# Kernel optimization log

Measured on AMD Instinct MI355X. Metric: run time of the kernel, lower is better.

The kernel has to match this reference:

```python
import jax, jax.numpy as jnp
import numpy as np

EPS = 1e-06

def rmsnorm(x, w):
    x32 = x.astype(jnp.float32)
    var = jnp.mean(x32 * x32, axis=-1, keepdims=True)
    return w * (x32 * jax.lax.rsqrt(var + EPS)).astype(x.dtype)

def setup_inputs() -> dict:
    B, T, C = 16, 256, 16
    token_dim, text_dim = 1024, 512
    key = jax.random.key(0)
    ks = jax.random.split(key, 8)
    token_embeds = jax.random.normal(ks[0], (B, T, token_dim), dtype=jnp.float32)
    char_embeds = jax.random.normal(ks[1], (B, T, C, text_dim), dtype=jnp.float32)
    filler_embed = jax.random.normal(ks[2], (text_dim,), dtype=jnp.float32)
    mask = jax.random.randint(ks[3], (B, T, C), 0, 2).astype(bool)
    mask = mask.at[0].set(True)  # force max valid count == T*C (static output shape)
    token_ids_mask = jnp.ones((B, T), dtype=bool)
    # xavier-uniform-ish weights
    def xav(k, fan_out, fan_in, gain=1.0):
        lim = gain * np.sqrt(6.0 / (fan_in + fan_out))
        return jax.random.uniform(k, (fan_out, fan_in), jnp.float32, -lim, lim)
    W_down = xav(ks[4], text_dim, token_dim)
    W_proj = xav(ks[5], 3, text_dim, gain=0.2)
    W_fusion = xav(ks[6], text_dim, text_dim)
    w_pre = jnp.ones((token_dim,), jnp.float32)
    w_tok = jnp.ones((text_dim,), jnp.float32)
    w_char = jnp.ones((text_dim,), jnp.float32)
    return {"token_embeds": token_embeds, "token_ids_mask": token_ids_mask,
            "char_embeds": char_embeds, "char_ids_mask": mask,
            "filler_embed": filler_embed, "w_pre": w_pre, "w_tok": w_tok,
            "w_char": w_char, "W_down": W_down, "W_proj": W_proj,
            "W_fusion": W_fusion, "max_valid_chars": T * C}

def reference(token_embeds, token_ids_mask, char_embeds, char_ids_mask,
              filler_embed, w_pre, w_tok, w_char, W_down, W_proj, W_fusion,
              max_valid_chars):
    B, T, C, d = char_embeds.shape
    MV = int(max_valid_chars)
    tok = rmsnorm(token_embeds, w_pre)                       # [B,T,token_dim]
    feats = rmsnorm(jnp.einsum('btk,dk->btd', tok, W_down), w_tok)  # [B,T,d]
    params = jnp.einsum('btd,pd->btp', jax.nn.silu(feats), W_proj)  # [B,T,3]
    scale = params[..., 0][:, :, None, None]                 # [B,T,1,1]
    shift = params[..., 1][:, :, None, None]
    gate = jax.nn.sigmoid(params[..., 2][:, :, None, None])
    cn = rmsnorm(char_embeds, w_char)                        # [B,T,C,d]
    fused = jnp.einsum('btcd,ed->btce', jax.nn.silu(cn * (1.0 + scale) + shift), W_fusion)
    fused = gate * fused + (1.0 - gate) * cn                 # [B,T,C,d]
    flat = fused.reshape(B, T * C, d)
    m = char_ids_mask.reshape(B, T * C).astype(jnp.int32)
    pos = jnp.cumsum(m, axis=1) - 1                          # dest within row
    offs = jnp.arange(B, dtype=jnp.int32)[:, None] * MV
    idx = jnp.where(m > 0, offs + pos, B * MV)               # invalid -> dump slot
    buf = jnp.broadcast_to(filler_embed, (B * MV + 1, d))
    buf = buf.at[idx.reshape(-1)].set(flat.reshape(-1, d))
    return buf[: B * MV].reshape(B, MV, d)
```

## Files before the change

kernel.cpp:

```cpp
#include <hip/hip_runtime.h>
#include <cstdint>
#include <cstddef>

#define EPS 1e-6f

typedef short bf16x8 __attribute__((ext_vector_type(8)));
typedef float f32x4  __attribute__((ext_vector_type(4)));

__device__ __forceinline__ short f2bf(float x) {
    uint32_t u = __builtin_bit_cast(uint32_t, x);
    return (short)((u + 0x7FFFu + ((u >> 16) & 1u)) >> 16);
}

__global__ __launch_bounds__(1024) void k_scan(const void* __restrict__ maskp,
                                               int* __restrict__ v_list,
                                               int* __restrict__ counts) {
    __shared__ int wtot[16];
    __shared__ int woff[16];
    __shared__ int mode_s;
    const int tid = threadIdx.x, lane = tid & 63, wave = tid >> 6;
    const int b = blockIdx.x;

    if (tid == 0) mode_s = 0;
    __syncthreads();
    {
        const int bad = (((const uint32_t*)maskp)[tid & 1023] > 1u) ? 1 : 0;
        if (bad) mode_s = 1;
    }
    __syncthreads();
    const int byte_mode = mode_s;

    int f0, f1, f2, f3;
    if (byte_mode) {
        const uint32_t v = ((const uint32_t*)maskp)[(b << 10) + tid];
        f0 = (v & 0x000000ffu) != 0;
        f1 = (v & 0x0000ff00u) != 0;
        f2 = (v & 0x00ff0000u) != 0;
        f3 = (v & 0xff000000u) != 0;
    } else {
        const uint4 v = ((const uint4*)maskp)[(b << 10) + tid];
        f0 = v.x != 0; f1 = v.y != 0; f2 = v.z != 0; f3 = v.w != 0;
    }
    const int c = f0 + f1 + f2 + f3;

    int incl = c;
#pragma unroll
    for (int off = 1; off < 64; off <<= 1) {
        const int n = __shfl_up(incl, off);
        if (lane >= off) incl += n;
    }
    if (lane == 63) wtot[wave] = incl;
    __syncthreads();
    if (tid == 0) {
        int run = 0;
#pragma unroll
        for (int wv = 0; wv < 16; ++wv) { woff[wv] = run; run += wtot[wv]; }
        counts[b] = run;
    }
    __syncthreads();

    int base = woff[wave] + incl - c;
    const int i0 = tid * 4;
    int* vl = v_list + (b << 12);
    if (f0) vl[base++] = i0;
    if (f1) vl[base++] = i0 + 1;
    if (f2) vl[base++] = i0 + 2;
    if (f3) vl[base++] = i0 + 3;
}

__global__ __launch_bounds__(256) void k_conv2(const float* __restrict__ srcA,
                                               short* __restrict__ dstA, int n4a,
                                               const float* __restrict__ srcB,
                                               short* __restrict__ dstB, int n4b) {
    const int gid = blockIdx.x * 256 + threadIdx.x;
    const float* s;
    short* d;
    int i;
    if (gid < n4a) { s = srcA; d = dstA; i = gid; }
    else {
        i = gid - n4a;
        if (i >= n4b) return;
        s = srcB; d = dstB;
    }
    const float4 v = ((const float4*)s)[i];
    short4 o;
    o.x = f2bf(v.x); o.y = f2bf(v.y); o.z = f2bf(v.z); o.w = f2bf(v.w);
    ((short4*)d)[i] = o;
}

__global__ __launch_bounds__(256) void k_tokprep(const float* __restrict__ tokens,
                                                 const float* __restrict__ w_pre,
                                                 short* __restrict__ tokbf) {
    const int tid = threadIdx.x, lane = tid & 63, wave = tid >> 6;
    const int row = blockIdx.x * 4 + wave;
    const float* xp = tokens + (size_t)row * 1024 + lane * 16;
    float4 x[4];
#pragma unroll
    for (int q = 0; q < 4; ++q) x[q] = *(const float4*)&xp[q * 4];
    float ss = 0.f;
#pragma unroll
    for (int q = 0; q < 4; ++q)
        ss += x[q].x * x[q].x + x[q].y * x[q].y + x[q].z * x[q].z + x[q].w * x[q].w;
#pragma unroll
    for (int off = 32; off > 0; off >>= 1) ss += __shfl_down(ss, off);
    ss = __shfl(ss, 0);
    const float r = rsqrtf(ss * (1.0f / 1024.0f) + EPS);
    const float* wp = w_pre + lane * 16;
    short* op = tokbf + (size_t)row * 1024 + lane * 16;
#pragma unroll
    for (int h = 0; h < 2; ++h) {
        bf16x8 o;
#pragma unroll
        for (int q = 0; q < 2; ++q) {
            const float4 wv = *(const float4*)&wp[h * 8 + q * 4];
            const float4 xv = x[h * 2 + q];
            o[q * 4 + 0] = f2bf(xv.x * wv.x * r);
            o[q * 4 + 1] = f2bf(xv.y * wv.y * r);
            o[q * 4 + 2] = f2bf(xv.z * wv.z * r);
            o[q * 4 + 3] = f2bf(xv.w * wv.w * r);
        }
        *(bf16x8*)&op[h * 8] = o;
    }
}

__global__ __launch_bounds__(256) void k_gemm_tok(const short* __restrict__ tokbf,
                                                  const short* __restrict__ Wdbf,
                                                  float* __restrict__ feats) {
    __shared__ short As[128 * 32];
    __shared__ short Bs[128 * 32];
    const int tid = threadIdx.x, lane = tid & 63, w = tid >> 6;
    const int kt = blockIdx.x >> 7;
    const int mt = (blockIdx.x >> 2) & 31, nt = blockIdx.x & 3;
    const int wm = w >> 1, wn = w & 1;
    const int kbase = kt * 512;
    const short* hA = tokbf + (size_t)mt * 128 * 1024;
    const short* wB = Wdbf + (size_t)nt * 128 * 1024;

    f32x4 acc[4][4];
#pragma unroll
    for (int mi = 0; mi < 4; ++mi)
#pragma unroll
        for (int ni = 0; ni < 4; ++ni) acc[mi][ni] = (f32x4)0.f;

    const int rA = lane & 15, q8 = (lane >> 4) * 8;
    for (int kk = 0; kk < 512; kk += 32) {
#pragma unroll
        for (int q = 0; q < 2; ++q) {
            const int cid = (w * 2 + q) * 64 + lane;
            const int r = cid >> 2, kc = cid & 3;
            const size_t go = (size_t)r * 1024 + kbase + kk + kc * 8;
            __builtin_amdgcn_global_load_lds(
                (const __attribute__((address_space(1))) uint32_t*)(hA + go),
                (__attribute__((address_space(3))) uint32_t*)&As[(w * 2 + q) * 512], 16, 0, 0);
            __builtin_amdgcn_global_load_lds(
                (const __attribute__((address_space(1))) uint32_t*)(wB + go),
                (__attribute__((address_space(3))) uint32_t*)&Bs[(w * 2 + q) * 512], 16, 0, 0);
        }
        __syncthreads();
        bf16x8 af[4], bfr[4];
#pragma unroll
        for (int mi = 0; mi < 4; ++mi)
            af[mi] = *(const bf16x8*)&As[(wm * 64 + mi * 16 + rA) * 32 + q8];
#pragma unroll
        for (int ni = 0; ni < 4; ++ni)
            bfr[ni] = *(const bf16x8*)&Bs[(wn * 64 + ni * 16 + rA) * 32 + q8];
#pragma unroll
        for (int mi = 0; mi < 4; ++mi)
#pragma unroll
            for (int ni = 0; ni < 4; ++ni)
                acc[mi][ni] = __builtin_amdgcn_mfma_f32_16x16x32_bf16(af[mi], bfr[ni], acc[mi][ni], 0, 0, 0);
        __syncthreads();
    }
    float* fo = feats + (size_t)kt * 4096 * 512;
    const int rowb = mt * 128 + wm * 64 + (lane >> 4) * 4;
    const int colb = nt * 128 + wn * 64 + (lane & 15);
#pragma unroll
    for (int mi = 0; mi < 4; ++mi)
#pragma unroll
        for (int ni = 0; ni < 4; ++ni)
#pragma unroll
            for (int rg = 0; rg < 4; ++rg)
                fo[(size_t)(rowb + mi * 16 + rg) * 512 + colb + ni * 16] = acc[mi][ni][rg];
}

__global__ __launch_bounds__(64) void k_params(
    const float* __restrict__ feats_pre, const float* __restrict__ w_tok,
    const float* __restrict__ W_proj, float* __restrict__ params) {
    const int tk = blockIdx.x;
    const int lane = threadIdx.x;
    const int d0 = lane * 8;
    const float* fp0 = feats_pre + (size_t)tk * 512 + d0;
    const float* fp1 = fp0 + (size_t)4096 * 512;
    const float4 a0 = *(const float4*)&fp0[0];
    const float4 a1 = *(const float4*)&fp0[4];
    const float4 b0 = *(const float4*)&fp1[0];
    const float4 b1 = *(const float4*)&fp1[4];
    const float4 f0 = make_float4(a0.x + b0.x, a0.y + b0.y, a0.z + b0.z, a0.w + b0.w);
    const float4 f1 = make_float4(a1.x + b1.x, a1.y + b1.y, a1.z + b1.z, a1.w + b1.w);
    float ss = f0.x * f0.x + f0.y * f0.y + f0.z * f0.z + f0.w * f0.w
             + f1.x * f1.x + f1.y * f1.y + f1.z * f1.z + f1.w * f1.w;
#pragma unroll
    for (int off = 32; off > 0; off >>= 1) ss += __shfl_down(ss, off);
    ss = __shfl(ss, 0);
    const float rms = rsqrtf(ss * (1.0f / 512.0f) + EPS);

    const float4 wt0 = *(const float4*)&w_tok[d0];
    const float4 wt1 = *(const float4*)&w_tok[d0 + 4];
    float fv[8] = {f0.x, f0.y, f0.z, f0.w, f1.x, f1.y, f1.z, f1.w};
    float wv[8] = {wt0.x, wt0.y, wt0.z, wt0.w, wt1.x, wt1.y, wt1.z, wt1.w};
    float s[8];
#pragma unroll
    for (int j = 0; j < 8; ++j) {
        const float v = fv[j] * wv[j] * rms;
        s[j] = v / (1.0f + expf(-v));
    }
    float p[3];
#pragma unroll
    for (int q = 0; q < 3; ++q) {
        const float* Wp = W_proj + (size_t)q * 512 + d0;
        const float4 a = *(const float4*)&Wp[0];
        const float4 c = *(const float4*)&Wp[4];
        p[q] = s[0] * a.x + s[1] * a.y + s[2] * a.z + s[3] * a.w
             + s[4] * c.x + s[5] * c.y + s[6] * c.z + s[7] * c.w;
#pragma unroll
        for (int off = 32; off > 0; off >>= 1) p[q] += __shfl_down(p[q], off);
    }
    if (lane == 0) {
        float* po = params + (size_t)tk * 4;
        po[0] = 1.0f + p[0];
        po[1] = p[1];
        po[2] = 1.0f / (1.0f + expf(-p[2]));
    }
}

__global__ __launch_bounds__(256) void k_prep(
    const float* __restrict__ chars, const float* __restrict__ w_char,
    const float* __restrict__ params, const int* __restrict__ v_list,
    const int* __restrict__ counts, short* __restrict__ hb,
    float* __restrict__ rms_l, float* __restrict__ g_l) {
    const int tid = threadIdx.x, lane = tid & 63, wave = tid >> 6;
    const int b = blockIdx.x >> 10;
    const int j = (blockIdx.x & 1023) * 4 + wave;
    const int cnt = counts[b];
    const int cpad = (cnt + 127) & ~127;
    if (j >= cpad) return;
    short* hrow = hb + ((size_t)(b << 12) + j) * 512 + lane * 8;
    if (j >= cnt) {
        *(bf16x8*)hrow = (bf16x8)0;
        return;
    }
    const int i = v_list[(b << 12) + j];
    const float* xp = chars + ((size_t)(b << 12) + i) * 512 + lane * 8;
    const float4 x0 = *(const float4*)&xp[0];
    const float4 x1 = *(const float4*)&xp[4];
    float ss = x0.x * x0.x + x0.y * x0.y + x0.z * x0.z + x0.w * x0.w
             + x1.x * x1.x + x1.y * x1.y + x1.z * x1.z + x1.w * x1.w;
#pragma unroll
    for (int off = 32; off > 0; off >>= 1) ss += __shfl_down(ss, off);
    ss = __shfl(ss, 0);
    const float rms = rsqrtf(ss * (1.0f / 512.0f) + EPS);
    const float* pp = params + (size_t)((b << 8) + (i >> 4)) * 4;
    const float s1 = pp[0], sh = pp[1], g = pp[2];
    const float4 w0 = *(const float4*)&w_char[lane * 8];
    const float4 w1 = *(const float4*)&w_char[lane * 8 + 4];
    float xv[8] = {x0.x, x0.y, x0.z, x0.w, x1.x, x1.y, x1.z, x1.w};
    float wv[8] = {w0.x, w0.y, w0.z, w0.w, w1.x, w1.y, w1.z, w1.w};
    bf16x8 o;
#pragma unroll
    for (int q = 0; q < 8; ++q) {
        const float cn = wv[q] * xv[q] * rms;
        const float a = cn * s1 + sh;
        o[q] = f2bf(a / (1.0f + expf(-a)));
    }
    *(bf16x8*)hrow = o;
    if (lane == 0) {
        rms_l[(b << 12) + j] = rms;
        g_l[(b << 12) + j] = g;
    }
}

__global__ __launch_bounds__(256) void k_gemm_fus(
    const short* __restrict__ hb, const short* __restrict__ Wbf,
    const float* __restrict__ chars, const float* __restrict__ w_char,
    const float* __restrict__ rms_l, const float* __restrict__ g_l,
    const int* __restrict__ v_list, const int* __restrict__ counts,
    const float* __restrict__ filler, float* __restrict__ out) {
    __shared__ short As[128 * 32];
    __shared__ short Bs[128 * 32];
    __shared__ float g_s[128], rms_s[128];
    __shared__ int idx_s[128];
    const int tid = threadIdx.x, lane = tid & 63, w = tid >> 6;
    const int b = blockIdx.x >> 7;
    const int mt = (blockIdx.x >> 2) & 31;
    const int nt = blockIdx.x & 3;
    const int cnt = counts[b];
    const int row0 = mt * 128;
    if (row0 >= cnt) {
        const int colb = nt * 128;
        const float4 f = ((const float4*)(filler + colb))[tid & 31];
        float* o0 = out + ((size_t)(b << 12) + row0) * 512 + colb + (tid & 31) * 4;
#pragma unroll
        for (int r = (tid >> 5); r < 128; r += 8)
            *(float4*)&o0[(size_t)r * 512] = f;
        return;
    }
    const int wm = w >> 1, wn = w & 1;

    if (tid < 128) {
        const int j = row0 + tid;
        const bool valid = j < cnt;
        idx_s[tid] = valid ? v_list[(b << 12) + j] : 0;
        g_s[tid]   = valid ? g_l[(b << 12) + j] : 0.f;
        rms_s[tid] = valid ? rms_l[(b << 12) + j] : 0.f;
    }

    const short* hA = hb + ((size_t)(b << 12) + row0) * 512;
    const short* wB = Wbf + (size_t)nt * 128 * 512;

    f32x4 acc[4][4];
#pragma unroll
    for (int mi = 0; mi < 4; ++mi)
#pragma unroll
        for (int ni = 0; ni < 4; ++ni) acc[mi][ni] = (f32x4)0.f;

    const int rA = lane & 15, q8 = (lane >> 4) * 8;
    for (int kk = 0; kk < 512; kk += 32) {
#pragma unroll
        for (int q = 0; q < 2; ++q) {
            const int cid = (w * 2 + q) * 64 + lane;
            const int r = cid >> 2, kc = cid & 3;
            const size_t go = (size_t)r * 512 + kk + kc * 8;
            __builtin_amdgcn_global_load_lds(
                (const __attribute__((address_space(1))) uint32_t*)(hA + go),
                (__attribute__((address_space(3))) uint32_t*)&As[(w * 2 + q) * 512], 16, 0, 0);
            __builtin_amdgcn_global_load_lds(
                (const __attribute__((address_space(1))) uint32_t*)(wB + go),
                (__attribute__((address_space(3))) uint32_t*)&Bs[(w * 2 + q) * 512], 16, 0, 0);
        }
        __syncthreads();
        bf16x8 af[4], bfr[4];
#pragma unroll
        for (int mi = 0; mi < 4; ++mi)
            af[mi] = *(const bf16x8*)&As[(wm * 64 + mi * 16 + rA) * 32 + q8];
#pragma unroll
        for (int ni = 0; ni < 4; ++ni)
            bfr[ni] = *(const bf16x8*)&Bs[(wn * 64 + ni * 16 + rA) * 32 + q8];
#pragma unroll
        for (int mi = 0; mi < 4; ++mi)
#pragma unroll
            for (int ni = 0; ni < 4; ++ni)
                acc[mi][ni] = __builtin_amdgcn_mfma_f32_16x16x32_bf16(af[mi], bfr[ni], acc[mi][ni], 0, 0, 0);
        __syncthreads();
    }

    const int colb = nt * 128 + wn * 64 + (lane & 15);
    float wcv[4];
#pragma unroll
    for (int ni = 0; ni < 4; ++ni) wcv[ni] = w_char[colb + ni * 16];
#pragma unroll
    for (int mi = 0; mi < 4; ++mi) {
#pragma unroll
        for (int rg = 0; rg < 4; ++rg) {
            const int jl = wm * 64 + mi * 16 + (lane >> 4) * 4 + rg;
            const int j = row0 + jl;
            const size_t orow = ((size_t)(b << 12) + j) * 512;
            if (j < cnt) {
                const float g = g_s[jl], rm = rms_s[jl];
                const size_t xrow = ((size_t)(b << 12) + idx_s[jl]) * 512;
#pragma unroll
                for (int ni = 0; ni < 4; ++ni) {
                    const int col = colb + ni * 16;
                    const float x = chars[xrow + col];
                    const float cn = wcv[ni] * x * rm;
                    out[orow + col] = g * acc[mi][ni][rg] + (1.0f - g) * cn;
                }
            } else {
#pragma unroll
                for (int ni = 0; ni < 4; ++ni) {
                    const int col = colb + ni * 16;
                    out[orow + col] = filler[col];
                }
            }
        }
    }
}

extern "C" void kernel_launch(void* const* d_in, const int* in_sizes, int n_in,
                              void* d_out, int out_size, void* d_ws, size_t ws_size,
                              hipStream_t stream) {
    const float* tokens = (const float*)d_in[0];
    const float* chars  = (const float*)d_in[2];
    const void*  cmask  = d_in[3];
    const float* filler = (const float*)d_in[4];
    const float* w_pre  = (const float*)d_in[5];
    const float* w_tok  = (const float*)d_in[6];
    const float* w_char = (const float*)d_in[7];
    const float* W_down = (const float*)d_in[8];
    const float* W_proj = (const float*)d_in[9];
    const float* W_fus  = (const float*)d_in[10];
    float* out = (float*)d_out;

    float* feats_pre = (float*)d_ws;
    float* params    = feats_pre + (size_t)2 * 4096 * 512;
    int*   counts    = (int*)(params + (size_t)4096 * 4);
    int*   v_list    = counts + 16;
    float* rms_l     = (float*)(v_list + 65536);
    float* g_l       = rms_l + 65536;
    short* Wbf       = (short*)(g_l + 65536);
    short* hb        = Wbf + (size_t)512 * 512;
    short* tokbf     = hb + (size_t)16 * 4096 * 512;
    short* Wdbf      = tokbf + (size_t)4096 * 1024;

    k_scan<<<16, 1024, 0, stream>>>(cmask, v_list, counts);
    k_conv2<<<768, 256, 0, stream>>>(W_fus, Wbf, 65536, W_down, Wdbf, 131072);
    k_tokprep<<<1024, 256, 0, stream>>>(tokens, w_pre, tokbf);
    k_gemm_tok<<<256, 256, 0, stream>>>(tokbf, Wdbf, feats_pre);
    k_params<<<4096, 64, 0, stream>>>(feats_pre, w_tok, W_proj, params);
    k_prep<<<16384, 256, 0, stream>>>(chars, w_char, params, v_list, counts, hb, rms_l, g_l);
    k_gemm_fus<<<2048, 256, 0, stream>>>(hb, Wbf, chars, w_char, rms_l, g_l, v_list, counts, filler, out);
}
```

Baseline: 339.8 us.

## Merge front kernels, swizzle GEMM LDS tiles, remap fusion blocks, use nontemporal stores

Folds the mask scan, weight bf16 conversion and token RMSNorm into one launch, cutting two kernel launches. It also adds an XOR swizzle to the LDS tile layout in both GEMMs to reduce bank conflicts on fragment reads. The fusion GEMM's block index is remapped so blocks are interleaved across XCDs, and output/filler writes become nontemporal stores to avoid cache pollution. The scan now uses 256 threads with 16 elements each, and params gets an explicit zero in its fourth slot.

```diff
diff --git a/kernel.cpp b/kernel.cpp
--- a/kernel.cpp
+++ b/kernel.cpp
@@ -12,114 +12,111 @@
     return (short)((u + 0x7FFFu + ((u >> 16) & 1u)) >> 16);
 }
 
-__global__ __launch_bounds__(1024) void k_scan(const void* __restrict__ maskp,
-                                               int* __restrict__ v_list,
-                                               int* __restrict__ counts) {
-    __shared__ int wtot[16];
-    __shared__ int woff[16];
-    __shared__ int mode_s;
-    const int tid = threadIdx.x, lane = tid & 63, wave = tid >> 6;
-    const int b = blockIdx.x;
-
-    if (tid == 0) mode_s = 0;
-    __syncthreads();
-    {
-        const int bad = (((const uint32_t*)maskp)[tid & 1023] > 1u) ? 1 : 0;
-        if (bad) mode_s = 1;
-    }
-    __syncthreads();
-    const int byte_mode = mode_s;
-
-    int f0, f1, f2, f3;
-    if (byte_mode) {
-        const uint32_t v = ((const uint32_t*)maskp)[(b << 10) + tid];
-        f0 = (v & 0x000000ffu) != 0;
-        f1 = (v & 0x0000ff00u) != 0;
-        f2 = (v & 0x00ff0000u) != 0;
-        f3 = (v & 0xff000000u) != 0;
+__global__ __launch_bounds__(256) void k_front(
+    const void* __restrict__ maskp, int* __restrict__ v_list, int* __restrict__ counts,
+    const float* __restrict__ Wf, short* __restrict__ Wfbf,
+    const float* __restrict__ Wd, short* __restrict__ Wdbf,
+    const float* __restrict__ tokens, const float* __restrict__ w_pre,
+    short* __restrict__ tokbf) {
+    const int blk = blockIdx.x, tid = threadIdx.x;
+    if (blk < 16) {
+        __shared__ int wtot[4], woff[4];
+        __shared__ int mode_s;
+        const int b = blk, lane = tid & 63, wave = tid >> 6;
+        if (tid == 0) mode_s = 0;
+        __syncthreads();
+        {
+            int bad = 0;
+#pragma unroll
+            for (int q = 0; q < 4; ++q)
+                bad |= (((const uint32_t*)maskp)[q * 256 + tid] > 1u) ? 1 : 0;
+            if (bad) mode_s = 1;
+        }
+        __syncthreads();
+        int f[16];
+        if (mode_s) {
+            const uint4 v = ((const uint4*)maskp)[(b << 8) + tid];
+            const uint32_t ws[4] = {v.x, v.y, v.z, v.w};
+#pragma unroll
+            for (int q = 0; q < 4; ++q) {
+                f[q * 4 + 0] = (ws[q] & 0x000000ffu) != 0;
+                f[q * 4 + 1] = (ws[q] & 0x0000ff00u) != 0;
+                f[q * 4 + 2] = (ws[q] & 0x00ff0000u) != 0;
+                f[q * 4 + 3] = (ws[q] & 0xff000000u) != 0;
+            }
+        } else {
+            const uint4* mp = (const uint4*)maskp + ((size_t)b << 10) + tid * 4;
+#pragma unroll
+            for (int q = 0; q < 4; ++q) {
+                const uint4 v = mp[q];
+                f[q * 4 + 0] = v.x != 0; f[q * 4 + 1] = v.y != 0;
+                f[q * 4 + 2] = v.z != 0; f[q * 4 + 3] = v.w != 0;
+            }
+        }
+        int c = 0;
+#pragma unroll
+        for (int q = 0; q < 16; ++q) c += f[q];
+        int incl = c;
+#pragma unroll
+        for (int off = 1; off < 64; off <<= 1) {
+            const int n = __shfl_up(incl, off);
+            if (lane >= off) incl += n;
+        }
+        if (lane == 63) wtot[wave] = incl;
+        __syncthreads();
+        if (tid == 0) {
+            int run = 0;
+#pragma unroll
+            for (int wv = 0; wv < 4; ++wv) { woff[wv] = run; run += wtot[wv]; }
+            counts[b] = run;
+        }
+        __syncthreads();
+        int base = woff[wave] + incl - c;
+        int* vl = v_list + (b << 12);
+        const int i0 = tid * 16;
+#pragma unroll
+        for (int q = 0; q < 16; ++q)
+            if (f[q]) vl[base++] = i0 + q;
+    } else if (blk < 784) {
+        const int gid = (blk - 16) * 256 + tid;
+        const float* s; short* d; int i;
+        if (gid < 65536) { s = Wf; d = Wfbf; i = gid; }
+        else             { s = Wd; d = Wdbf; i = gid - 65536; }
+        const float4 v = ((const float4*)s)[i];
+        short4 o;
+        o.x = f2bf(v.x); o.y = f2bf(v.y); o.z = f2bf(v.z); o.w = f2bf(v.w);
+        ((short4*)d)[i] = o;
     } else {
-        const uint4 v = ((const uint4*)maskp)[(b << 10) + tid];
-        f0 = v.x != 0; f1 = v.y != 0; f2 = v.z != 0; f3 = v.w != 0;
-    }
-    const int c = f0 + f1 + f2 + f3;
-
-    int incl = c;
-#pragma unroll
-    for (int off = 1; off < 64; off <<= 1) {
-        const int n = __shfl_up(incl, off);
-        if (lane >= off) incl += n;
-    }
-    if (lane == 63) wtot[wave] = incl;
-    __syncthreads();
-    if (tid == 0) {
-        int run = 0;
-#pragma unroll
-        for (int wv = 0; wv < 16; ++wv) { woff[wv] = run; run += wtot[wv]; }
-        counts[b] = run;
-    }
-    __syncthreads();
-
-    int base = woff[wave] + incl - c;
-    const int i0 = tid * 4;
-    int* vl = v_list + (b << 12);
-    if (f0) vl[base++] = i0;
-    if (f1) vl[base++] = i0 + 1;
-    if (f2) vl[base++] = i0 + 2;
-    if (f3) vl[base++] = i0 + 3;
-}
-
-__global__ __launch_bounds__(256) void k_conv2(const float* __restrict__ srcA,
-                                               short* __restrict__ dstA, int n4a,
-                                               const float* __restrict__ srcB,
-                                               short* __restrict__ dstB, int n4b) {
-    const int gid = blockIdx.x * 256 + threadIdx.x;
-    const float* s;
-    short* d;
-    int i;
-    if (gid < n4a) { s = srcA; d = dstA; i = gid; }
-    else {
-        i = gid - n4a;
-        if (i >= n4b) return;
-        s = srcB; d = dstB;
-    }
-    const float4 v = ((const float4*)s)[i];
-    short4 o;
-    o.x = f2bf(v.x); o.y = f2bf(v.y); o.z = f2bf(v.z); o.w = f2bf(v.w);
-    ((short4*)d)[i] = o;
-}
-
-__global__ __launch_bounds__(256) void k_tokprep(const float* __restrict__ tokens,
-                                                 const float* __restrict__ w_pre,
-                                                 short* __restrict__ tokbf) {
-    const int tid = threadIdx.x, lane = tid & 63, wave = tid >> 6;
-    const int row = blockIdx.x * 4 + wave;
-    const float* xp = tokens + (size_t)row * 1024 + lane * 16;
-    float4 x[4];
-#pragma unroll
-    for (int q = 0; q < 4; ++q) x[q] = *(const float4*)&xp[q * 4];
-    float ss = 0.f;
-#pragma unroll
-    for (int q = 0; q < 4; ++q)
-        ss += x[q].x * x[q].x + x[q].y * x[q].y + x[q].z * x[q].z + x[q].w * x[q].w;
-#pragma unroll
-    for (int off = 32; off > 0; off >>= 1) ss += __shfl_down(ss, off);
-    ss = __shfl(ss, 0);
-    const float r = rsqrtf(ss * (1.0f / 1024.0f) + EPS);
-    const float* wp = w_pre + lane * 16;
-    short* op = tokbf + (size_t)row * 1024 + lane * 16;
-#pragma unroll
-    for (int h = 0; h < 2; ++h) {
-        bf16x8 o;
-#pragma unroll
-        for (int q = 0; q < 2; ++q) {
-            const float4 wv = *(const float4*)&wp[h * 8 + q * 4];
-            const float4 xv = x[h * 2 + q];
-            o[q * 4 + 0] = f2bf(xv.x * wv.x * r);
-            o[q * 4 + 1] = f2bf(xv.y * wv.y * r);
-            o[q * 4 + 2] = f2bf(xv.z * wv.z * r);
-            o[q * 4 + 3] = f2bf(xv.w * wv.w * r);
-        }
-        *(bf16x8*)&op[h * 8] = o;
+        const int lane = tid & 63, wave = tid >> 6;
+        const int row = (blk - 784) * 4 + wave;
+        const float* xp = tokens + (size_t)row * 1024 + lane * 16;
+        float4 x[4];
+#pragma unroll
+        for (int q = 0; q < 4; ++q) x[q] = *(const float4*)&xp[q * 4];
+        float ss = 0.f;
+#pragma unroll
+        for (int q = 0; q < 4; ++q)
+            ss += x[q].x * x[q].x + x[q].y * x[q].y + x[q].z * x[q].z + x[q].w * x[q].w;
+#pragma unroll
+        for (int off = 32; off > 0; off >>= 1) ss += __shfl_down(ss, off);
+        ss = __shfl(ss, 0);
+        const float r = rsqrtf(ss * (1.0f / 1024.0f) + EPS);
+        const float* wp = w_pre + lane * 16;
+        short* op = tokbf + (size_t)row * 1024 + lane * 16;
+#pragma unroll
+        for (int h = 0; h < 2; ++h) {
+            bf16x8 o;
+#pragma unroll
+            for (int q = 0; q < 2; ++q) {
+                const float4 wv = *(const float4*)&wp[h * 8 + q * 4];
+                const float4 xv = x[h * 2 + q];
+                o[q * 4 + 0] = f2bf(xv.x * wv.x * r);
+                o[q * 4 + 1] = f2bf(xv.y * wv.y * r);
+                o[q * 4 + 2] = f2bf(xv.z * wv.z * r);
+                o[q * 4 + 3] = f2bf(xv.w * wv.w * r);
+            }
+            *(bf16x8*)&op[h * 8] = o;
+        }
     }
 }
 
@@ -142,13 +139,14 @@
 #pragma unroll
         for (int ni = 0; ni < 4; ++ni) acc[mi][ni] = (f32x4)0.f;
 
-    const int rA = lane & 15, q8 = (lane >> 4) * 8;
+    const int rA = lane & 15, ch = lane >> 4;
     for (int kk = 0; kk < 512; kk += 32) {
 #pragma unroll
         for (int q = 0; q < 2; ++q) {
             const int cid = (w * 2 + q) * 64 + lane;
             const int r = cid >> 2, kc = cid & 3;
-            const size_t go = (size_t)r * 1024 + kbase + kk + kc * 8;
+            const int kcs = kc ^ ((r >> 1) & 3);
+            const size_t go = (size_t)r * 1024 + kbase + kk + kcs * 8;
             __builtin_amdgcn_global_load_lds(
                 (const __attribute__((address_space(1))) uint32_t*)(hA + go),
                 (__attribute__((address_space(3))) uint32_t*)&As[(w * 2 + q) * 512], 16, 0, 0);
@@ -159,11 +157,15 @@
         __syncthreads();
         bf16x8 af[4], bfr[4];
 #pragma unroll
-        for (int mi = 0; mi < 4; ++mi)
-            af[mi] = *(const bf16x8*)&As[(wm * 64 + mi * 16 + rA) * 32 + q8];
-#pragma unroll
-        for (int ni = 0; ni < 4; ++ni)
-            bfr[ni] = *(const bf16x8*)&Bs[(wn * 64 + ni * 16 + rA) * 32 + q8];
+        for (int mi = 0; mi < 4; ++mi) {
+            const int row = wm * 64 + mi * 16 + rA;
+            af[mi] = *(const bf16x8*)&As[row * 32 + ((ch ^ ((row >> 1) & 3)) << 3)];
+        }
+#pragma unroll
+        for (int ni = 0; ni < 4; ++ni) {
+            const int row = wn * 64 + ni * 16 + rA;
+            bfr[ni] = *(const bf16x8*)&Bs[row * 32 + ((ch ^ ((row >> 1) & 3)) << 3)];
+        }
 #pragma unroll
         for (int mi = 0; mi < 4; ++mi)
 #pragma unroll
@@ -230,6 +232,7 @@
         po[0] = 1.0f + p[0];
         po[1] = p[1];
         po[2] = 1.0f / (1.0f + expf(-p[2]));
+        po[3] = 0.f;
     }
 }
 
@@ -285,25 +288,26 @@
     const float* __restrict__ rms_l, const float* __restrict__ g_l,
     const int* __restrict__ v_list, const int* __restrict__ counts,
     const float* __restrict__ filler, float* __restrict__ out) {
+    const int wg = (blockIdx.x & 7) * 256 + (blockIdx.x >> 3);
+    const int b = wg >> 7;
+    const int mt = (wg >> 2) & 31;
+    const int nt = wg & 3;
+    const int tid = threadIdx.x, lane = tid & 63, w = tid >> 6;
+    const int cnt = counts[b];
+    const int row0 = mt * 128;
+    if (row0 >= cnt) {
+        const int colb0 = nt * 128;
+        const f32x4 f = *(const f32x4*)(filler + colb0 + (tid & 31) * 4);
+        float* o0 = out + ((size_t)(b << 12) + row0) * 512 + colb0 + (tid & 31) * 4;
+        for (int r = tid >> 5; r < 128; r += 8)
+            __builtin_nontemporal_store(f, (f32x4*)&o0[(size_t)r * 512]);
+        return;
+    }
+
     __shared__ short As[128 * 32];
     __shared__ short Bs[128 * 32];
     __shared__ float g_s[128], rms_s[128];
     __shared__ int idx_s[128];
-    const int tid = threadIdx.x, lane = tid & 63, w = tid >> 6;
-    const int b = blockIdx.x >> 7;
-    const int mt = (blockIdx.x >> 2) & 31;
-    const int nt = blockIdx.x & 3;
-    const int cnt = counts[b];
-    const int row0 = mt * 128;
-    if (row0 >= cnt) {
-        const int colb = nt * 128;
-        const float4 f = ((const float4*)(filler + colb))[tid & 31];
-        float* o0 = out + ((size_t)(b << 12) + row0) * 512 + colb + (tid & 31) * 4;
-#pragma unroll
-        for (int r = (tid >> 5); r < 128; r += 8)
-            *(float4*)&o0[(size_t)r * 512] = f;
-        return;
-    }
     const int wm = w >> 1, wn = w & 1;
 
     if (tid < 128) {
@@ -323,13 +327,14 @@
 #pragma unroll
         for (int ni = 0; ni < 4; ++ni) acc[mi][ni] = (f32x4)0.f;
 
-    const int rA = lane & 15, q8 = (lane >> 4) * 8;
+    const int rA = lane & 15, ch = lane >> 4;
     for (int kk = 0; kk < 512; kk += 32) {
 #pragma unroll
         for (int q = 0; q < 2; ++q) {
             const int cid = (w * 2 + q) * 64 + lane;
             const int r = cid >> 2, kc = cid & 3;
-            const size_t go = (size_t)r * 512 + kk + kc * 8;
+            const int kcs = kc ^ ((r >> 1) & 3);
+            const size_t go = (size_t)r * 512 + kk + kcs * 8;
             __builtin_amdgcn_global_load_lds(
                 (const __attribute__((address_space(1))) uint32_t*)(hA + go),
                 (__attribute__((address_space(3))) uint32_t*)&As[(w * 2 + q) * 512], 16, 0, 0);
@@ -340,11 +345,15 @@
         __syncthreads();
         bf16x8 af[4], bfr[4];
 #pragma unroll
-        for (int mi = 0; mi < 4; ++mi)
-            af[mi] = *(const bf16x8*)&As[(wm * 64 + mi * 16 + rA) * 32 + q8];
-#pragma unroll
-        for (int ni = 0; ni < 4; ++ni)
-            bfr[ni] = *(const bf16x8*)&Bs[(wn * 64 + ni * 16 + rA) * 32 + q8];
+        for (int mi = 0; mi < 4; ++mi) {
+            const int row = wm * 64 + mi * 16 + rA;
+            af[mi] = *(const bf16x8*)&As[row * 32 + ((ch ^ ((row >> 1) & 3)) << 3)];
+        }
+#pragma unroll
+        for (int ni = 0; ni < 4; ++ni) {
+            const int row = wn * 64 + ni * 16 + rA;
+            bfr[ni] = *(const bf16x8*)&Bs[row * 32 + ((ch ^ ((row >> 1) & 3)) << 3)];
+        }
 #pragma unroll
         for (int mi = 0; mi < 4; ++mi)
 #pragma unroll
@@ -372,13 +381,14 @@
                     const int col = colb + ni * 16;
                     const float x = chars[xrow + col];
                     const float cn = wcv[ni] * x * rm;
-                    out[orow + col] = g * acc[mi][ni][rg] + (1.0f - g) * cn;
+                    __builtin_nontemporal_store(g * acc[mi][ni][rg] + (1.0f - g) * cn,
+                                                &out[orow + col]);
                 }
             } else {
 #pragma unroll
                 for (int ni = 0; ni < 4; ++ni) {
                     const int col = colb + ni * 16;
-                    out[orow + col] = filler[col];
+                    __builtin_nontemporal_store(filler[col], &out[orow + col]);
                 }
             }
         }
@@ -411,11 +421,11 @@
     short* tokbf     = hb + (size_t)16 * 4096 * 512;
     short* Wdbf      = tokbf + (size_t)4096 * 1024;
 
-    k_scan<<<16, 1024, 0, stream>>>(cmask, v_list, counts);
-    k_conv2<<<768, 256, 0, stream>>>(W_fus, Wbf, 65536, W_down, Wdbf, 131072);
-    k_tokprep<<<1024, 256, 0, stream>>>(tokens, w_pre, tokbf);
+    k_front<<<1808, 256, 0, stream>>>(cmask, v_list, counts, W_fus, Wbf,
+                                      W_down, Wdbf, tokens, w_pre, tokbf);
     k_gemm_tok<<<256, 256, 0, stream>>>(tokbf, Wdbf, feats_pre);
     k_params<<<4096, 64, 0, stream>>>(feats_pre, w_tok, W_proj, params);
     k_prep<<<16384, 256, 0, stream>>>(chars, w_char, params, v_list, counts, hb, rms_l, g_l);
-    k_gemm_fus<<<2048, 256, 0, stream>>>(hb, Wbf, chars, w_char, rms_l, g_l, v_list, counts, filler, out);
-}
+    k_gemm_fus<<<2048, 256, 0, stream>>>(hb, Wbf, chars, w_char, rms_l, g_l,
+                                         v_list, counts, filler, out);
+}
```

New measurement: 326.3 us. 4.0% less time.
